# Optimization experiments

Measured on AMD Instinct MI355X. Metric: run time of the kernel, lower is better.

## Reference

```python
import jax, jax.numpy as jnp
import numpy as np

LBL = 20            # original label_size
T = LBL + 2         # +START/+STOP for CRF
START = T - 2
STOP = T - 1
B, S, V, E, H = 64, 256, 50000, 300, 256


def setup_inputs() -> dict:
    key = jax.random.key(0)
    ks = jax.random.split(key, 20)
    s = 0.05
    inp = {
        "word_input": jax.random.randint(ks[0], (B, S), 0, V),
        "input_mask": jnp.ones((B, S), dtype=jnp.int32),
        "labels": jax.random.randint(ks[1], (B, S), 0, LBL),
        "labels_token": jax.random.randint(ks[2], (B, S), 0, 2),
        "emb_table": jax.random.normal(ks[3], (V, E)) * s,
        # PyTorch LSTM gate order: i, f, g, o (stacked along dim 0 of W)
        "Wih_f": jax.random.normal(ks[4], (4 * H, E)) * s,
        "Whh_f": jax.random.normal(ks[5], (4 * H, H)) * s,
        "bih_f": jax.random.normal(ks[6], (4 * H,)) * s,
        "bhh_f": jax.random.normal(ks[7], (4 * H,)) * s,
        "Wih_b": jax.random.normal(ks[8], (4 * H, E)) * s,
        "Whh_b": jax.random.normal(ks[9], (4 * H, H)) * s,
        "bih_b": jax.random.normal(ks[10], (4 * H,)) * s,
        "bhh_b": jax.random.normal(ks[11], (4 * H,)) * s,
        "W_tag": jax.random.normal(ks[12], (T, 2 * H)) * s,
        "b_tag": jax.random.normal(ks[13], (T,)) * s,
        "W_tok": jax.random.normal(ks[14], (2, 2 * H)) * s,
        "b_tok": jax.random.normal(ks[15], (2,)) * s,
        "trans": jax.random.normal(ks[16], (T, T)) * 0.1,
    }
    return inp


def _lstm_dir(x, Wih, Whh, bih, bhh, reverse):
    # x: [B, S, E] -> hs: [B, S, H]
    b = x.shape[0]
    h0 = jnp.zeros((b, Whh.shape[1]), x.dtype)

    def step(carry, xt):
        h, c = carry
        g = xt @ Wih.T + bih + h @ Whh.T + bhh
        i, f, gg, o = jnp.split(g, 4, axis=-1)
        c = jax.nn.sigmoid(f) * c + jax.nn.sigmoid(i) * jnp.tanh(gg)
        h = jax.nn.sigmoid(o) * jnp.tanh(c)
        return (h, c), h

    _, hs = jax.lax.scan(step, (h0, h0), jnp.swapaxes(x, 0, 1), reverse=reverse)
    return jnp.swapaxes(hs, 0, 1)


def _crf_nll(feats, mask, tags, trans):
    # feats: [B,S,T], mask: [B,S] int, tags: [B,S]
    maskf = mask.astype(feats.dtype)
    feats_t = jnp.swapaxes(feats, 0, 1)  # [S,B,T]
    mask_t = jnp.swapaxes(mask, 0, 1)
    part0 = feats_t[0] + trans[START][None]  # [B,T]

    def step(part, inputs):
        ft, mt = inputs
        newp = jax.nn.logsumexp(part[:, :, None] + trans[None], axis=1) + ft
        return jnp.where(mt[:, None] > 0, newp, part), None

    part, _ = jax.lax.scan(step, part0, (feats_t[1:], mask_t[1:]))
    fwd = jax.nn.logsumexp(part + trans[:, STOP][None], axis=1).sum()

    prev = jnp.concatenate(
        [jnp.full((tags.shape[0], 1), START, dtype=tags.dtype), tags[:, :-1]], axis=1)
    emit = jnp.take_along_axis(feats, tags[:, :, None], axis=2)[:, :, 0]
    gold = ((emit + trans[prev, tags]) * maskf).sum()
    lengths = mask.sum(axis=1)
    last_tag = jnp.take_along_axis(tags, (lengths - 1)[:, None], axis=1)[:, 0]
    gold = gold + trans[last_tag, STOP].sum()
    return fwd - gold


def _viterbi(feats, mask, trans):
    feats_t = jnp.swapaxes(feats, 0, 1)
    mask_t = jnp.swapaxes(mask, 0, 1)
    vit0 = feats_t[0] + trans[START][None]  # [B,T]
    idT = jnp.arange(T)

    def step(vit, inputs):
        ft, mt = inputs
        sc = vit[:, :, None] + trans[None]       # [B, T_prev, T_cur]
        bp = jnp.argmax(sc, axis=1)
        newv = jnp.max(sc, axis=1) + ft
        vit = jnp.where(mt[:, None] > 0, newv, vit)
        bp = jnp.where(mt[:, None] > 0, bp, idT[None])  # identity at padding
        return vit, bp

    vit, bps = jax.lax.scan(step, vit0, (feats_t[1:], mask_t[1:]))  # bps: [S-1,B,T]
    final = vit + trans[:, STOP][None]
    score = jnp.max(final, axis=1)
    last = jnp.argmax(final, axis=1)

    def back(tag, bp):
        prev = jnp.take_along_axis(bp, tag[:, None], axis=1)[:, 0]
        return prev, prev

    _, prevs = jax.lax.scan(back, last, bps, reverse=True)  # [S-1,B]
    tags = jnp.concatenate([prevs, last[None]], axis=0)      # [S,B]
    return score, jnp.swapaxes(tags, 0, 1)


def reference(word_input, input_mask, labels, labels_token, emb_table,
              Wih_f, Whh_f, bih_f, bhh_f, Wih_b, Whh_b, bih_b, bhh_b,
              W_tag, b_tag, W_tok, b_tok, trans):
    x = emb_table[word_input]                                  # [B,S,E]
    x = x * input_mask[:, :, None].astype(x.dtype)
    h_f = _lstm_dir(x, Wih_f, Whh_f, bih_f, bhh_f, reverse=False)
    h_b = _lstm_dir(x, Wih_b, Whh_b, bih_b, bhh_b, reverse=True)
    output = jnp.concatenate([h_f, h_b], axis=-1)              # [B,S,2H]

    tag_feats = output @ W_tag.T + b_tag                       # [B,S,T]
    tok_logits = output @ W_tok.T + b_tok                      # [B,S,2]

    # token CE: active positions (mask==1) and ignore_index=0
    logp = jax.nn.log_softmax(tok_logits, axis=-1)
    ce = -jnp.take_along_axis(logp, labels_token[:, :, None], axis=2)[:, :, 0]
    w = ((input_mask == 1) & (labels_token != 0)).astype(ce.dtype)
    token_loss = (ce * w).sum() / jnp.maximum(w.sum(), 1.0)

    nll = _crf_nll(tag_feats, input_mask, labels, trans)
    scores, tag_seq = _viterbi(tag_feats, input_mask, trans)
    ans_loss = nll / word_input.shape[0] + token_loss
    return ans_loss, tag_seq
```

## Files before the change

### kernel.cpp

```cpp
#include <hip/hip_runtime.h>
#include <math.h>

typedef unsigned short u16;
typedef unsigned int u32;

#define NB 64
#define NS 256
#define NE 300
#define NH 256
#define NT 22
#define KPAD 304
#define NBS (NB*NS)
#define START_TAG 20
#define STOP_TAG 21

#define RKC 8
#define LDSC 9
#define SKC 47

typedef float f32x4 __attribute__((ext_vector_type(4)));

__device__ __forceinline__ float fsig(float x) {
    return 1.f / (1.f + expf(-x));
}

__global__ __launch_bounds__(128) void gather_ax(const int* __restrict__ word,
                                                 const int* __restrict__ mask,
                                                 const float* __restrict__ emb,
                                                 float* __restrict__ Ax) {
    int bs = blockIdx.x;
    int t = threadIdx.x;
    if (t >= 76) return;
    int w = word[bs];
    int m = mask[bs];
    f32x4 v = {0.f, 0.f, 0.f, 0.f};
    if (t < 75 && m != 0) v = *(const f32x4*)(emb + (size_t)w * NE + t * 4);
    *(f32x4*)(Ax + (size_t)bs * KPAD + t * 4) = v;
}

__global__ __launch_bounds__(64) void pack_wih(const float* __restrict__ Wf, const float* __restrict__ Wb,
                                               const float* __restrict__ bihf, const float* __restrict__ bhhf,
                                               const float* __restrict__ bihb, const float* __restrict__ bhhb,
                                               float* __restrict__ WihP, float* __restrict__ biasP) {
    int j = blockIdx.x & 1023;
    int dir = blockIdx.x >> 10;
    const float* W = dir ? Wb : Wf;
    for (int k = threadIdx.x; k < KPAD; k += 64)
        WihP[((size_t)dir * 1024 + j) * KPAD + k] = (k < NE) ? W[(size_t)j * NE + k] : 0.f;
    if (threadIdx.x == 0) {
        const float* b1 = dir ? bihb : bihf;
        const float* b2 = dir ? bhhb : bhhf;
        biasP[dir * 1024 + j] = b1[j] + b2[j];
    }
}

__global__ __launch_bounds__(256) void pack_wstream(const float* __restrict__ Whf,
                                                    const float* __restrict__ Whb,
                                                    float* __restrict__ Wst) {
    int idx = blockIdx.x * 256 + threadIdx.x;
    int tid = idx & 511;
    int r = (idx >> 9) & 1;
    int cc = (idx >> 10) % SKC;
    int dir = idx / (SKC * 1024);
    const float* W = dir ? Whb : Whf;
    int row = ((tid >= 256) ? 512 : 0) + (tid & 255) + r * 256;
    f32x4 v = *(const f32x4*)(W + (size_t)row * NH + 4 * (RKC + LDSC + cc));
    *((f32x4*)Wst + idx) = v;
}

__global__ __launch_bounds__(256) void gemm_xproj(const float* __restrict__ Ax,
                                                  const float* __restrict__ WihP,
                                                  const float* __restrict__ biasP,
                                                  float* __restrict__ Xp) {
    int m0 = blockIdx.x * 64;
    int n0 = blockIdx.y * 64;
    int dir = blockIdx.z;
    const float* Bsrc = WihP + (size_t)dir * 1024 * KPAD;
    __shared__ float Asm[16][68];
    __shared__ float Bsm[16][68];
    int tid = threadIdx.x;
    int r = tid >> 2;
    int c4 = (tid & 3) * 4;
    int ty = tid >> 4;
    int tx = tid & 15;
    float acc[4][4] = {};

    for (int ks = 0; ks < KPAD / 16; ++ks) {
        int k0 = ks * 16;
        f32x4 ga = *(const f32x4*)(Ax + (size_t)(m0 + r) * KPAD + k0 + c4);
        f32x4 gb = *(const f32x4*)(Bsrc + (size_t)(n0 + r) * KPAD + k0 + c4);
        __syncthreads();
#pragma unroll
        for (int j = 0; j < 4; ++j) {
            Asm[c4 + j][r] = ga[j];
            Bsm[c4 + j][r] = gb[j];
        }
        __syncthreads();
#pragma unroll
        for (int k = 0; k < 16; ++k) {
            f32x4 a4 = *(const f32x4*)&Asm[k][ty * 4];
            f32x4 b4 = *(const f32x4*)&Bsm[k][tx * 4];
#pragma unroll
            for (int i = 0; i < 4; ++i)
#pragma unroll
                for (int j = 0; j < 4; ++j)
                    acc[i][j] = fmaf(a4[i], b4[j], acc[i][j]);
        }
    }
    f32x4 bv = *(const f32x4*)(biasP + dir * 1024 + n0 + tx * 4);
#pragma unroll
    for (int i = 0; i < 4; ++i) {
        f32x4 o;
#pragma unroll
        for (int j = 0; j < 4; ++j) o[j] = acc[i][j] + bv[j];
        *(f32x4*)(Xp + ((size_t)dir * NBS + m0 + ty * 4 + i) * 1024 + n0 + tx * 4) = o;
    }
}

__global__ __launch_bounds__(512, 2) void lstm4(const float* __restrict__ Xp,
                                                const float* __restrict__ Whf,
                                                const float* __restrict__ Whb,
                                                const float* __restrict__ Wst,
                                                float* __restrict__ hbuf) {
    int bid = blockIdx.x;
    int dir = bid >> 6;
    int b = bid & 63;
    int tid = threadIdx.x;
    int g2 = tid >> 8;
    int j = tid & 255;
    __shared__ f32x4 wlds[2 * LDSC][512];
    __shared__ float h_sh[256];
    __shared__ float2 exch[256];

    const float* W = dir ? Whb : Whf;
    int row0 = (g2 ? 512 : 0) + j;
    int row1 = row0 + 256;
    const f32x4* w0 = (const f32x4*)(W + (size_t)row0 * NH);
    const f32x4* w1 = (const f32x4*)(W + (size_t)row1 * NH);
    const f32x4* ws = (const f32x4*)Wst + (size_t)dir * SKC * 1024;

    f32x4 wr0[RKC], wr1[RKC];
#pragma unroll
    for (int i = 0; i < RKC; ++i) { wr0[i] = w0[i]; wr1[i] = w1[i]; }
#pragma unroll
    for (int i = 0; i < LDSC; ++i) {
        wlds[i][tid] = w0[RKC + i];
        wlds[LDSC + i][tid] = w1[RKC + i];
    }

    const float* X = Xp + ((size_t)dir * NBS + (size_t)b * NS) * 1024;
    float* Hout = hbuf + ((size_t)dir * NBS + (size_t)b * NS) * NH;
    const f32x4* hs4 = (const f32x4*)h_sh;
    float c = 0.f;
    if (g2 == 0) h_sh[j] = 0.f;
    __syncthreads();

    for (int t = 0; t < NS; ++t) {
        int s = dir ? (NS - 1 - t) : t;
        float acc0 = X[(size_t)s * 1024 + row0];
        float acc1 = X[(size_t)s * 1024 + row1];
#pragma unroll 8
        for (int cc = 0; cc < SKC; ++cc) {
            f32x4 wa = ws[(size_t)(cc * 2 + 0) * 512 + tid];
            f32x4 wb = ws[(size_t)(cc * 2 + 1) * 512 + tid];
            f32x4 hq = hs4[RKC + LDSC + cc];
            acc0 = fmaf(wa[0], hq[0], fmaf(wa[1], hq[1], fmaf(wa[2], hq[2], fmaf(wa[3], hq[3], acc0))));
            acc1 = fmaf(wb[0], hq[0], fmaf(wb[1], hq[1], fmaf(wb[2], hq[2], fmaf(wb[3], hq[3], acc1))));
        }
#pragma unroll
        for (int i = 0; i < RKC; ++i) {
            f32x4 hq = hs4[i];
            acc0 = fmaf(wr0[i][0], hq[0], fmaf(wr0[i][1], hq[1], fmaf(wr0[i][2], hq[2], fmaf(wr0[i][3], hq[3], acc0))));
            acc1 = fmaf(wr1[i][0], hq[0], fmaf(wr1[i][1], hq[1], fmaf(wr1[i][2], hq[2], fmaf(wr1[i][3], hq[3], acc1))));
        }
#pragma unroll
        for (int i = 0; i < LDSC; ++i) {
            f32x4 wa = wlds[i][tid];
            f32x4 wb = wlds[LDSC + i][tid];
            f32x4 hq = hs4[RKC + i];
            acc0 = fmaf(wa[0], hq[0], fmaf(wa[1], hq[1], fmaf(wa[2], hq[2], fmaf(wa[3], hq[3], acc0))));
            acc1 = fmaf(wb[0], hq[0], fmaf(wb[1], hq[1], fmaf(wb[2], hq[2], fmaf(wb[3], hq[3], acc1))));
        }
        if (g2) exch[j] = make_float2(tanhf(acc0), fsig(acc1));
        __syncthreads();
        if (!g2) {
            float gi = fsig(acc0), gf = fsig(acc1);
            float2 go = exch[j];
            c = gf * c + gi * go.x;
            float h = go.y * tanhf(c);
            h_sh[j] = h;
            Hout[(size_t)s * NH + j] = h;
        }
        __syncthreads();
    }
}

__global__ __launch_bounds__(256) void feats_kernel(const float* __restrict__ hbuf,
                                                    const float* __restrict__ Wtag, const float* __restrict__ btag,
                                                    const float* __restrict__ Wtok, const float* __restrict__ btok,
                                                    const int* __restrict__ mask, const int* __restrict__ ltok,
                                                    float* __restrict__ feats,
                                                    float* __restrict__ ce_arr, float* __restrict__ cnt_arr) {
    int gw = (blockIdx.x * 256 + threadIdx.x) >> 6;
    int lane = threadIdx.x & 63;
    float ce = 0.f, cnt = 0.f;
    for (int i = 0; i < 8; ++i) {
        int bs = gw * 8 + i;
        size_t base = (lane < 32) ? ((size_t)bs * NH + lane * 8)
                                  : ((size_t)NBS * NH + (size_t)bs * NH + (lane - 32) * 8);
        f32x4 v0 = *(const f32x4*)(hbuf + base);
        f32x4 v1 = *(const f32x4*)(hbuf + base + 4);
        float vals[8] = {v0[0], v0[1], v0[2], v0[3], v1[0], v1[1], v1[2], v1[3]};
        float t0 = 0.f, t1 = 0.f;
        for (int u = 0; u < 24; ++u) {
            const float* wr = (u < NT) ? (Wtag + (size_t)u * 512) : (Wtok + (size_t)(u - NT) * 512);
            f32x4 w0 = *(const f32x4*)(wr + lane * 8);
            f32x4 w1 = *(const f32x4*)(wr + lane * 8 + 4);
            float d = vals[0] * w0[0] + vals[1] * w0[1] + vals[2] * w0[2] + vals[3] * w0[3]
                    + vals[4] * w1[0] + vals[5] * w1[1] + vals[6] * w1[2] + vals[7] * w1[3];
#pragma unroll
            for (int o = 32; o; o >>= 1) d += __shfl_xor(d, o);
            if (u < NT) {
                if (lane == 0) feats[(size_t)bs * 24 + u] = d + btag[u];
            } else if (u == NT) {
                t0 = d + btok[0];
            } else {
                t1 = d + btok[1];
            }
        }
        if (lane == 0) {
            float m = fmaxf(t0, t1);
            float lse = m + logf(expf(t0 - m) + expf(t1 - m));
            int lab = ltok[bs];
            int mk = mask[bs];
            if (mk == 1 && lab != 0) {
                ce += lse - (lab ? t1 : t0);
                cnt += 1.f;
            }
        }
    }
    if (lane == 0) { ce_arr[gw] = ce; cnt_arr[gw] = cnt; }
}

__global__ __launch_bounds__(64) void crf_kernel(const float* __restrict__ feats,
                                                 const int* __restrict__ mask,
                                                 const int* __restrict__ labels,
                                                 const float* __restrict__ trans,
                                                 float* __restrict__ contrib,
                                                 float* __restrict__ outtags) {
    int b = blockIdx.x, t = threadIdx.x;
    __shared__ float tr[NT * NT];
    __shared__ float part_sh[NT], vit_sh[NT];
    __shared__ float red[NT];
    __shared__ unsigned char bp[NS][NT];
    for (int i = t; i < NT * NT; i += 64) tr[i] = trans[i];
    __syncthreads();
    const float* F = feats + (size_t)b * NS * 24;
    const int* Mrow = mask + b * NS;
    const int* Lrow = labels + b * NS;
    float part = 0.f, vit = 0.f;
    if (t < NT) {
        part = F[t] + tr[START_TAG * NT + t];
        vit = part;
        part_sh[t] = part;
        vit_sh[t] = vit;
    }
    __syncthreads();
    for (int s = 1; s < NS; ++s) {
        float newp = part, newv = vit;
        int bi = t;
        if (t < NT) {
            float ft = F[s * 24 + t];
            float mx = -1e30f;
#pragma unroll
            for (int p = 0; p < NT; ++p) mx = fmaxf(mx, part_sh[p] + tr[p * NT + t]);
            float sm = 0.f;
#pragma unroll
            for (int p = 0; p < NT; ++p) sm += expf(part_sh[p] + tr[p * NT + t] - mx);
            float cp = mx + logf(sm) + ft;
            float bm = -1e30f;
            int bj = 0;
#pragma unroll
            for (int p = 0; p < NT; ++p) {
                float sc = vit_sh[p] + tr[p * NT + t];
                if (sc > bm) { bm = sc; bj = p; }
            }
            float cv = bm + ft;
            if (Mrow[s] > 0) { newp = cp; newv = cv; bi = bj; }
        }
        __syncthreads();
        if (t < NT) {
            part = newp; vit = newv;
            part_sh[t] = part; vit_sh[t] = vit;
            bp[s][t] = (unsigned char)bi;
        }
        __syncthreads();
    }
    float val = (t < NT) ? part + tr[t * NT + STOP_TAG] : -1e30f;
    float mx = val;
#pragma unroll
    for (int o = 32; o; o >>= 1) mx = fmaxf(mx, __shfl_xor(mx, o));
    float ex = (t < NT) ? expf(val - mx) : 0.f;
#pragma unroll
    for (int o = 32; o; o >>= 1) ex += __shfl_xor(ex, o);
    float fwd = mx + logf(ex);
    if (t < NT) red[t] = vit + tr[t * NT + STOP_TAG];
    __syncthreads();
    if (t == 0) {
        float bm = -1e30f;
        int bi = 0;
        for (int p = 0; p < NT; ++p)
            if (red[p] > bm) { bm = red[p]; bi = p; }
        int cur = bi;
        outtags[b * NS + NS - 1] = (float)cur;
        for (int s = NS - 1; s >= 1; --s) {
            cur = bp[s][cur];
            outtags[b * NS + s - 1] = (float)cur;
        }
    }
    float g = 0.f;
    int len = 0;
    for (int s = t; s < NS; s += 64) {
        int tg = Lrow[s];
        int pv = (s == 0) ? START_TAG : Lrow[s - 1];
        if (Mrow[s] > 0) {
            g += F[s * 24 + tg] + tr[pv * NT + tg];
            len += 1;
        }
    }
#pragma unroll
    for (int o = 32; o; o >>= 1) { g += __shfl_xor(g, o); len += __shfl_xor(len, o); }
    if (t == 0) {
        int lt = Lrow[len - 1];
        g += tr[lt * NT + STOP_TAG];
        contrib[b] = fwd - g;
    }
}

__global__ __launch_bounds__(256) void finalize_kernel(const float* __restrict__ contrib,
                                                       const float* __restrict__ ce_arr,
                                                       const float* __restrict__ cnt_arr,
                                                       float* __restrict__ out) {
    __shared__ float sA[256], sB[256], sC[256];
    int t = threadIdx.x;
    float a = (t < NB) ? contrib[t] : 0.f;
    float bb = 0.f, cc = 0.f;
    for (int i = t; i < 2048; i += 256) { bb += ce_arr[i]; cc += cnt_arr[i]; }
    sA[t] = a; sB[t] = bb; sC[t] = cc;
    __syncthreads();
    for (int o = 128; o; o >>= 1) {
        if (t < o) { sA[t] += sA[t + o]; sB[t] += sB[t + o]; sC[t] += sC[t + o]; }
        __syncthreads();
    }
    if (t == 0)
        out[0] = sA[0] / (float)NB + sB[0] / fmaxf(sC[0], 1.f);
}

extern "C" void kernel_launch(void* const* d_in, const int* in_sizes, int n_in,
                              void* d_out, int out_size, void* d_ws, size_t ws_size,
                              hipStream_t stream) {
    const int*   word   = (const int*)d_in[0];
    const int*   mask   = (const int*)d_in[1];
    const int*   labels = (const int*)d_in[2];
    const int*   ltok   = (const int*)d_in[3];
    const float* emb    = (const float*)d_in[4];
    const float* Wih_f  = (const float*)d_in[5];
    const float* Whh_f  = (const float*)d_in[6];
    const float* bih_f  = (const float*)d_in[7];
    const float* bhh_f  = (const float*)d_in[8];
    const float* Wih_b  = (const float*)d_in[9];
    const float* Whh_b  = (const float*)d_in[10];
    const float* bih_b  = (const float*)d_in[11];
    const float* bhh_b  = (const float*)d_in[12];
    const float* Wtag   = (const float*)d_in[13];
    const float* btag   = (const float*)d_in[14];
    const float* Wtok   = (const float*)d_in[15];
    const float* btok   = (const float*)d_in[16];
    const float* trans  = (const float*)d_in[17];
    float* out = (float*)d_out;

    char* ws = (char*)d_ws;
    size_t off = 0;
    auto alloc = [&](size_t bytes) { size_t r = off; off += (bytes + 255) & ~(size_t)255; return r; };
    float* Ax     = (float*)(ws + alloc((size_t)NBS * KPAD * 4));
    float* WihP   = (float*)(ws + alloc((size_t)2 * 1024 * KPAD * 4));
    float* biasP  = (float*)(ws + alloc((size_t)2 * 1024 * 4));
    float* Wst    = (float*)(ws + alloc((size_t)2 * SKC * 1024 * 16));
    float* Xp     = (float*)(ws + alloc((size_t)2 * NBS * 1024 * 4));
    float* hbuf   = (float*)(ws + alloc((size_t)2 * NBS * NH * 4));
    float* feats  = (float*)(ws + alloc((size_t)NBS * 24 * 4));
    float* contrib= (float*)(ws + alloc((size_t)NB * 4));
    float* ce_arr = (float*)(ws + alloc((size_t)2048 * 4));
    float* cnt_arr= (float*)(ws + alloc((size_t)2048 * 4));

    gather_ax<<<NBS, 128, 0, stream>>>(word, mask, emb, Ax);
    pack_wih<<<2048, 64, 0, stream>>>(Wih_f, Wih_b, bih_f, bhh_f, bih_b, bhh_b, WihP, biasP);
    pack_wstream<<<(2 * SKC * 1024) / 256, 256, 0, stream>>>(Whh_f, Whh_b, Wst);
    gemm_xproj<<<dim3(NBS / 64, 1024 / 64, 2), 256, 0, stream>>>(Ax, WihP, biasP, Xp);
    lstm4<<<128, 512, 0, stream>>>(Xp, Whh_f, Whh_b, Wst, hbuf);
    feats_kernel<<<512, 256, 0, stream>>>(hbuf, Wtag, btag, Wtok, btok, mask, ltok, feats, ce_arr, cnt_arr);
    crf_kernel<<<NB, 64, 0, stream>>>(feats, mask, labels, trans, contrib, out + 1);
    finalize_kernel<<<1, 256, 0, stream>>>(contrib, ce_arr, cnt_arr, out);
}
```

Before: 2.477 ms.

## Use one thread per gate row in LSTM recurrence and enlarge GEMM tile

The recurrent LSTM kernel now runs 1024 threads per block, one per gate row, instead of 512 threads each computing two rows. This halves the serial dot-product work per thread on each timestep. More of Whh is kept in registers (20 chunks) and less is streamed from global memory, with the streamed layout repacked to match. The input-projection GEMM tile grows to 128x64 with 8x4 outputs per thread for more reuse. The cost is higher register pressure per thread, a wider barrier, and a three-way exchange of gate values through shared memory.

```diff
diff --git a/kernel.cpp b/kernel.cpp
--- a/kernel.cpp
+++ b/kernel.cpp
@@ -14,9 +14,9 @@
 #define START_TAG 20
 #define STOP_TAG 21
 
-#define RKC 8
+#define RKC 20
 #define LDSC 9
-#define SKC 47
+#define SKC 35
 
 typedef float f32x4 __attribute__((ext_vector_type(4)));
 
@@ -58,12 +58,11 @@
                                                     const float* __restrict__ Whb,
                                                     float* __restrict__ Wst) {
     int idx = blockIdx.x * 256 + threadIdx.x;
-    int tid = idx & 511;
-    int r = (idx >> 9) & 1;
-    int cc = (idx >> 10) % SKC;
     int dir = idx / (SKC * 1024);
+    int r = idx % (SKC * 1024);
+    int cc = r >> 10;
+    int row = r & 1023;
     const float* W = dir ? Whb : Whf;
-    int row = ((tid >= 256) ? 512 : 0) + (tid & 255) + r * 256;
     f32x4 v = *(const f32x4*)(W + (size_t)row * NH + 4 * (RKC + LDSC + cc));
     *((f32x4*)Wst + idx) = v;
 }
@@ -72,122 +71,119 @@
                                                   const float* __restrict__ WihP,
                                                   const float* __restrict__ biasP,
                                                   float* __restrict__ Xp) {
-    int m0 = blockIdx.x * 64;
+    int m0 = blockIdx.x * 128;
     int n0 = blockIdx.y * 64;
     int dir = blockIdx.z;
     const float* Bsrc = WihP + (size_t)dir * 1024 * KPAD;
-    __shared__ float Asm[16][68];
+    __shared__ float Asm[16][132];
     __shared__ float Bsm[16][68];
     int tid = threadIdx.x;
-    int r = tid >> 2;
-    int c4 = (tid & 3) * 4;
+    int arow = tid >> 1;
+    int acol = (tid & 1) * 8;
+    int brow = tid >> 2;
+    int bcol = (tid & 3) * 4;
     int ty = tid >> 4;
     int tx = tid & 15;
-    float acc[4][4] = {};
+    float acc[8][4] = {};
 
     for (int ks = 0; ks < KPAD / 16; ++ks) {
         int k0 = ks * 16;
-        f32x4 ga = *(const f32x4*)(Ax + (size_t)(m0 + r) * KPAD + k0 + c4);
-        f32x4 gb = *(const f32x4*)(Bsrc + (size_t)(n0 + r) * KPAD + k0 + c4);
+        f32x4 ga0 = *(const f32x4*)(Ax + (size_t)(m0 + arow) * KPAD + k0 + acol);
+        f32x4 ga1 = *(const f32x4*)(Ax + (size_t)(m0 + arow) * KPAD + k0 + acol + 4);
+        f32x4 gb = *(const f32x4*)(Bsrc + (size_t)(n0 + brow) * KPAD + k0 + bcol);
         __syncthreads();
 #pragma unroll
         for (int j = 0; j < 4; ++j) {
-            Asm[c4 + j][r] = ga[j];
-            Bsm[c4 + j][r] = gb[j];
+            Asm[acol + j][arow] = ga0[j];
+            Asm[acol + 4 + j][arow] = ga1[j];
+            Bsm[bcol + j][brow] = gb[j];
         }
         __syncthreads();
 #pragma unroll
         for (int k = 0; k < 16; ++k) {
-            f32x4 a4 = *(const f32x4*)&Asm[k][ty * 4];
+            f32x4 a0 = *(const f32x4*)&Asm[k][ty * 8];
+            f32x4 a1 = *(const f32x4*)&Asm[k][ty * 8 + 4];
             f32x4 b4 = *(const f32x4*)&Bsm[k][tx * 4];
 #pragma unroll
             for (int i = 0; i < 4; ++i)
 #pragma unroll
-                for (int j = 0; j < 4; ++j)
-                    acc[i][j] = fmaf(a4[i], b4[j], acc[i][j]);
+                for (int j = 0; j < 4; ++j) {
+                    acc[i][j] = fmaf(a0[i], b4[j], acc[i][j]);
+                    acc[i + 4][j] = fmaf(a1[i], b4[j], acc[i + 4][j]);
+                }
         }
     }
     f32x4 bv = *(const f32x4*)(biasP + dir * 1024 + n0 + tx * 4);
 #pragma unroll
-    for (int i = 0; i < 4; ++i) {
+    for (int i = 0; i < 8; ++i) {
         f32x4 o;
 #pragma unroll
         for (int j = 0; j < 4; ++j) o[j] = acc[i][j] + bv[j];
-        *(f32x4*)(Xp + ((size_t)dir * NBS + m0 + ty * 4 + i) * 1024 + n0 + tx * 4) = o;
-    }
-}
-
-__global__ __launch_bounds__(512, 2) void lstm4(const float* __restrict__ Xp,
-                                                const float* __restrict__ Whf,
-                                                const float* __restrict__ Whb,
-                                                const float* __restrict__ Wst,
-                                                float* __restrict__ hbuf) {
+        *(f32x4*)(Xp + ((size_t)dir * NBS + m0 + ty * 8 + i) * 1024 + n0 + tx * 4) = o;
+    }
+}
+
+__global__ __launch_bounds__(1024, 4) void lstm5(const float* __restrict__ Xp,
+                                                 const float* __restrict__ Whf,
+                                                 const float* __restrict__ Whb,
+                                                 const float* __restrict__ Wst,
+                                                 float* __restrict__ hbuf) {
     int bid = blockIdx.x;
     int dir = bid >> 6;
     int b = bid & 63;
     int tid = threadIdx.x;
-    int g2 = tid >> 8;
+    int gate = tid >> 8;
     int j = tid & 255;
-    __shared__ f32x4 wlds[2 * LDSC][512];
+    __shared__ f32x4 wlds[LDSC][1024];
     __shared__ float h_sh[256];
-    __shared__ float2 exch[256];
+    __shared__ float exch[3][256];
 
     const float* W = dir ? Whb : Whf;
-    int row0 = (g2 ? 512 : 0) + j;
-    int row1 = row0 + 256;
-    const f32x4* w0 = (const f32x4*)(W + (size_t)row0 * NH);
-    const f32x4* w1 = (const f32x4*)(W + (size_t)row1 * NH);
+    const f32x4* wrow = (const f32x4*)(W + (size_t)tid * NH);
     const f32x4* ws = (const f32x4*)Wst + (size_t)dir * SKC * 1024;
 
-    f32x4 wr0[RKC], wr1[RKC];
-#pragma unroll
-    for (int i = 0; i < RKC; ++i) { wr0[i] = w0[i]; wr1[i] = w1[i]; }
-#pragma unroll
-    for (int i = 0; i < LDSC; ++i) {
-        wlds[i][tid] = w0[RKC + i];
-        wlds[LDSC + i][tid] = w1[RKC + i];
-    }
+    f32x4 wr[RKC];
+#pragma unroll
+    for (int i = 0; i < RKC; ++i) wr[i] = wrow[i];
+#pragma unroll
+    for (int i = 0; i < LDSC; ++i) wlds[i][tid] = wrow[RKC + i];
 
     const float* X = Xp + ((size_t)dir * NBS + (size_t)b * NS) * 1024;
     float* Hout = hbuf + ((size_t)dir * NBS + (size_t)b * NS) * NH;
     const f32x4* hs4 = (const f32x4*)h_sh;
     float c = 0.f;
-    if (g2 == 0) h_sh[j] = 0.f;
+    if (gate == 0) h_sh[j] = 0.f;
     __syncthreads();
 
     for (int t = 0; t < NS; ++t) {
         int s = dir ? (NS - 1 - t) : t;
-        float acc0 = X[(size_t)s * 1024 + row0];
-        float acc1 = X[(size_t)s * 1024 + row1];
-#pragma unroll 8
+        float acc = X[(size_t)s * 1024 + tid];
+#pragma unroll 5
         for (int cc = 0; cc < SKC; ++cc) {
-            f32x4 wa = ws[(size_t)(cc * 2 + 0) * 512 + tid];
-            f32x4 wb = ws[(size_t)(cc * 2 + 1) * 512 + tid];
+            f32x4 wv = ws[(size_t)cc * 1024 + tid];
             f32x4 hq = hs4[RKC + LDSC + cc];
-            acc0 = fmaf(wa[0], hq[0], fmaf(wa[1], hq[1], fmaf(wa[2], hq[2], fmaf(wa[3], hq[3], acc0))));
-            acc1 = fmaf(wb[0], hq[0], fmaf(wb[1], hq[1], fmaf(wb[2], hq[2], fmaf(wb[3], hq[3], acc1))));
+            acc = fmaf(wv[0], hq[0], fmaf(wv[1], hq[1], fmaf(wv[2], hq[2], fmaf(wv[3], hq[3], acc))));
         }
 #pragma unroll
         for (int i = 0; i < RKC; ++i) {
             f32x4 hq = hs4[i];
-            acc0 = fmaf(wr0[i][0], hq[0], fmaf(wr0[i][1], hq[1], fmaf(wr0[i][2], hq[2], fmaf(wr0[i][3], hq[3], acc0))));
-            acc1 = fmaf(wr1[i][0], hq[0], fmaf(wr1[i][1], hq[1], fmaf(wr1[i][2], hq[2], fmaf(wr1[i][3], hq[3], acc1))));
+            acc = fmaf(wr[i][0], hq[0], fmaf(wr[i][1], hq[1], fmaf(wr[i][2], hq[2], fmaf(wr[i][3], hq[3], acc))));
         }
 #pragma unroll
         for (int i = 0; i < LDSC; ++i) {
-            f32x4 wa = wlds[i][tid];
-            f32x4 wb = wlds[LDSC + i][tid];
+            f32x4 wv = wlds[i][tid];
             f32x4 hq = hs4[RKC + i];
-            acc0 = fmaf(wa[0], hq[0], fmaf(wa[1], hq[1], fmaf(wa[2], hq[2], fmaf(wa[3], hq[3], acc0))));
-            acc1 = fmaf(wb[0], hq[0], fmaf(wb[1], hq[1], fmaf(wb[2], hq[2], fmaf(wb[3], hq[3], acc1))));
-        }
-        if (g2) exch[j] = make_float2(tanhf(acc0), fsig(acc1));
-        __syncthreads();
-        if (!g2) {
-            float gi = fsig(acc0), gf = fsig(acc1);
-            float2 go = exch[j];
-            c = gf * c + gi * go.x;
-            float h = go.y * tanhf(c);
+            acc = fmaf(wv[0], hq[0], fmaf(wv[1], hq[1], fmaf(wv[2], hq[2], fmaf(wv[3], hq[3], acc))));
+        }
+        if (gate) exch[gate - 1][j] = (gate == 2) ? tanhf(acc) : fsig(acc);
+        __syncthreads();
+        if (!gate) {
+            float gi = fsig(acc);
+            float gf = exch[0][j];
+            float gg = exch[1][j];
+            float oo = exch[2][j];
+            c = gf * c + gi * gg;
+            float h = oo * tanhf(c);
             h_sh[j] = h;
             Hout[(size_t)s * NH + j] = h;
         }
@@ -396,8 +392,8 @@
     gather_ax<<<NBS, 128, 0, stream>>>(word, mask, emb, Ax);
     pack_wih<<<2048, 64, 0, stream>>>(Wih_f, Wih_b, bih_f, bhh_f, bih_b, bhh_b, WihP, biasP);
     pack_wstream<<<(2 * SKC * 1024) / 256, 256, 0, stream>>>(Whh_f, Whh_b, Wst);
-    gemm_xproj<<<dim3(NBS / 64, 1024 / 64, 2), 256, 0, stream>>>(Ax, WihP, biasP, Xp);
-    lstm4<<<128, 512, 0, stream>>>(Xp, Whh_f, Whh_b, Wst, hbuf);
+    gemm_xproj<<<dim3(NBS / 128, 1024 / 64, 2), 256, 0, stream>>>(Ax, WihP, biasP, Xp);
+    lstm5<<<128, 1024, 0, stream>>>(Xp, Whh_f, Whh_b, Wst, hbuf);
     feats_kernel<<<512, 256, 0, stream>>>(hbuf, Wtag, btag, Wtok, btok, mask, ltok, feats, ce_arr, cnt_arr);
     crf_kernel<<<NB, 64, 0, stream>>>(feats, mask, labels, trans, contrib, out + 1);
     finalize_kernel<<<1, 256, 0, stream>>>(contrib, ce_arr, cnt_arr, out);
```

Measured after the change: 2.246 ms. -9.3%, faster.
